# Kernel optimization log

Hardware: AMD Instinct MI355X
Metric: run time of the kernel (lower is better)

The kernel has to match this reference:

```python
import jax, jax.numpy as jnp
import numpy as np
from jax import lax

B, N, M = 4, 16384, 512
RADIUS2 = 4.0        # radius=2 (hard-coded in forward), compare squared distances
BALL_K = 64          # k=64 hard-coded in forward
KNN_K = 9            # opt.node_knn_k_1
SIGMA_LB = 0.001     # opt.loss_sigma_lower_bound

_DIMS = [("conv1", 6, 64), ("conv2", 64, 64), ("conv3", 64, 64),
         ("conv4", 128, 128), ("conv5", 128, 128),
         ("knnb1", 131, 256), ("knnb2", 256, 256), ("knnb3", 256, 256),
         ("knna1", 512, 512), ("knna2", 512, 512),
         ("mlp1", 640, 512), ("mlp2", 512, 256)]


def setup_inputs() -> dict:
    key = jax.random.key(0)
    ks = jax.random.split(key, 6)
    inp = {
        "x": jax.random.normal(ks[0], (B, 3, N), jnp.float32),
        "sn": jax.random.normal(ks[1], (B, 3, N), jnp.float32),
        "node": jax.random.normal(ks[2], (B, 3, M), jnp.float32),
    }
    for i, (name, cin, cout) in enumerate(_DIMS):
        k = jax.random.fold_in(ks[3], i)
        inp[name + "_w"] = jax.random.normal(k, (cout, cin), jnp.float32) * np.float32(1.0 / np.sqrt(cin))
        inp[name + "_b"] = jnp.zeros((cout,), jnp.float32)
    inp["mlp3_w"] = jax.random.normal(ks[4], (4, 256), jnp.float32) * np.float32(1e-4)  # .normal_(0, 0.0001)
    inp["mlp3_b"] = jnp.zeros((4,), jnp.float32)
    return inp


def _conv(f, w, b, act=True):
    # 1x1 conv over (B,C,M) or (B,C,M,K): channel matmul + bias (+relu)
    y = jnp.einsum('oc,bc...->bo...', w, f) + b.reshape((1, -1) + (1,) * (f.ndim - 2))
    return jax.nn.relu(y) if act else y


def _sqdist(a, b):
    # a: (B,3,Ma), b: (B,3,Nb) -> (B,Ma,Nb) squared euclidean distances
    aa = jnp.sum(a * a, axis=1)
    bb = jnp.sum(b * b, axis=1)
    ab = jnp.einsum('bcm,bcn->bmn', a, b)
    return aa[:, :, None] + bb[:, None, :] - 2.0 * ab


def _gather(feat, idx):
    # feat: (B,C,Nb), idx: (B,Mq,K) -> (B,C,Mq,K)
    Bq, C, _ = feat.shape
    _, Mq, K = idx.shape
    flat = jnp.broadcast_to(idx.reshape(Bq, 1, Mq * K), (Bq, C, Mq * K))
    return jnp.take_along_axis(feat, flat, axis=2).reshape(Bq, C, Mq, K)


def _ball_query(sqd, radius2, k):
    # first k point indices (in original order) with dist<radius, padded by the first hit
    n = sqd.shape[2]
    mask = sqd < radius2
    keyi = jnp.where(mask, jnp.arange(n, dtype=jnp.int32)[None, None, :], jnp.int32(n))
    _, idx = lax.top_k(-keyi, k)  # k smallest keys == first k in-ball indices
    count = jnp.sum(mask, axis=2, keepdims=True)
    return jnp.where(jnp.arange(k)[None, None, :] < count, idx, idx[:, :, :1])


def reference(x, sn, node,
              conv1_w, conv1_b, conv2_w, conv2_b, conv3_w, conv3_b,
              conv4_w, conv4_b, conv5_w, conv5_b,
              knnb1_w, knnb1_b, knnb2_w, knnb2_b, knnb3_w, knnb3_b,
              knna1_w, knna1_b, knna2_w, knna2_b,
              mlp1_w, mlp1_b, mlp2_w, mlp2_b, mlp3_w, mlp3_b):
    x_aug = jnp.concatenate([x, sn], axis=1)                      # (B,6,N)
    idx = _ball_query(_sqdist(node, x), RADIUS2, BALL_K)          # (B,M,64)
    xb = _gather(x_aug, idx)                                      # (B,6,M,64)
    xb = jnp.concatenate([xb[:, :3] - node[:, :, :, None], xb[:, 3:]], axis=1)
    f = _conv(_conv(_conv(xb, conv1_w, conv1_b), conv2_w, conv2_b), conv3_w, conv3_b)
    fmax = jnp.max(f, axis=3, keepdims=True)
    f = jnp.concatenate([f, jnp.broadcast_to(fmax, f.shape)], axis=1)
    f = _conv(_conv(f, conv4_w, conv4_b), conv5_w, conv5_b)
    feat1 = jnp.max(f, axis=3)                                    # (B,128,M)

    # GeneralKNNFusionModule: query=node, database=node, x=feat1, K=KNN_K
    _, knn_idx = lax.top_k(-_sqdist(node, node), KNN_K)           # (B,M,K) nearest nodes
    coords = _gather(node, knn_idx) - node[:, :, :, None]         # (B,3,M,K)
    g = jnp.concatenate([coords, _gather(feat1, knn_idx)], axis=1)  # (B,131,M,K)
    g = _conv(_conv(_conv(g, knnb1_w, knnb1_b), knnb2_w, knnb2_b), knnb3_w, knnb3_b)
    gmax = jnp.max(g, axis=3, keepdims=True)
    g = jnp.concatenate([g, jnp.broadcast_to(gmax, g.shape)], axis=1)
    g = _conv(_conv(g, knna1_w, knna1_b), knna2_w, knna2_b)
    feat2 = jnp.max(g, axis=3)                                    # (B,512,M)

    h = jnp.concatenate([feat1, feat2], axis=1)                   # (B,640,M)
    h = _conv(_conv(h, mlp1_w, mlp1_b), mlp2_w, mlp2_b)
    ksig = _conv(h, mlp3_w, mlp3_b, act=False)                    # (B,4,M)
    keypoints = ksig[:, :3] + node
    sigmas = jax.nn.softplus(ksig[:, 3]) + SIGMA_LB
    return node, keypoints, sigmas
```

## Files before the change

kernel.cpp:

```cpp
#include <hip/hip_runtime.h>

typedef unsigned short u16;
typedef unsigned int u32;
typedef __bf16 bf16x8 __attribute__((ext_vector_type(8)));
typedef float floatx4 __attribute__((ext_vector_type(4)));
typedef unsigned short u16x8 __attribute__((ext_vector_type(8)));
typedef unsigned int u32x4 __attribute__((ext_vector_type(4)));

static constexpr int B_ = 4;
static constexpr int N_ = 16384;
static constexpr int M_ = 512;

__device__ __forceinline__ u16 f2bf(float f) {
    u32 u = __float_as_uint(f);
    u32 r = (u + 0x7fffu + ((u >> 16) & 1u)) >> 16;
    return (u16)r;
}
__device__ __forceinline__ float bf2f(u16 x) {
    return __uint_as_float(((u32)x) << 16);
}
__device__ __forceinline__ u32 pack2(float a, float b) {
    return (u32)f2bf(a) | ((u32)f2bf(b) << 16);
}

struct WConvArgs { const float* src[12]; };

__global__ __launch_bounds__(256) void prep_kernel(
    const float* __restrict__ node, int* __restrict__ knn,
    WConvArgs wa, u16* __restrict__ Wbf) {
    int bid = blockIdx.x;
    int tid = threadIdx.x, wave = tid >> 6, lane = tid & 63;

    if (bid < 512) {
        int bm = bid * 4 + wave;
        int b = bm >> 9, m = bm & 511;
        const float* nb = node + (size_t)b * 3 * M_;
        float nx = nb[m], ny = nb[M_ + m], nz = nb[2 * M_ + m];
        float aa = nx * nx + ny * ny + nz * nz;
        float dist[8];
        int didx[8];
#pragma unroll
        for (int i = 0; i < 8; ++i) {
            int n = lane + i * 64;
            float px = nb[n], py = nb[M_ + n], pz = nb[2 * M_ + n];
            float bb = px * px + py * py + pz * pz;
            float ab = nx * px + ny * py + nz * pz;
            dist[i] = aa + bb - 2.0f * ab;
            didx[i] = n;
        }
        for (int r = 0; r < 9; ++r) {
            float bv = dist[0]; int bi = didx[0]; int bslot = 0;
#pragma unroll
            for (int i = 1; i < 8; ++i) {
                if (dist[i] < bv || (dist[i] == bv && didx[i] < bi)) {
                    bv = dist[i]; bi = didx[i]; bslot = i;
                }
            }
            float rv = bv; int ri = bi;
            for (int off = 32; off > 0; off >>= 1) {
                float ov = __shfl_down(rv, off);
                int   oi = __shfl_down(ri, off);
                if (ov < rv || (ov == rv && oi < ri)) { rv = ov; ri = oi; }
            }
            ri = __shfl(ri, 0);
            if (lane == 0) knn[(size_t)bm * 9 + r] = ri;
            if (bi == ri) dist[bslot] = 3.0e38f;
        }
    } else {
        const int CI[12] = {6, 64, 64, 128, 128, 131, 256, 256, 512, 512, 640, 512};
        const int KP[12] = {32, 64, 64, 128, 128, 160, 256, 256, 512, 512, 640, 512};
        const int OFF[13] = {0, 2048, 6144, 10240, 26624, 43008, 83968, 149504,
                             215040, 477184, 739328, 1067008, 1198080};
        int e = (bid - 512) * 256 + tid;
        int w = 0;
        while (e >= OFF[w + 1]) ++w;
        int local = e - OFF[w];
        int kp = KP[w];
        int co = local / kp, k = local - co * kp;
        float v = 0.0f;
        if (w == 5) {
            if (k < 3) v = wa.src[5][(size_t)co * 131 + k];
            else if (k >= 8 && k < 136) v = wa.src[5][(size_t)co * 131 + (k - 5)];
        } else if (k < CI[w]) {
            v = wa.src[w][(size_t)co * CI[w] + k];
        }
        Wbf[e] = f2bf(v);
    }
}

static constexpr int RS = 136;

__device__ __forceinline__ bf16x8 ldsA(const u16* act, int rf, int l15, int quad, int ks) {
    return *(const bf16x8*)(act + (rf * 16 + l15) * RS + ks * 32 + quad * 8);
}
__device__ __forceinline__ bf16x8 ldW(const u16* W, int ks, int l15, int quad, int kstride) {
    return *(const bf16x8*)(W + (size_t)l15 * kstride + ks * 32 + quad * 8);
}

__global__ __launch_bounds__(256, 4) void fused_stage1_kernel(
    const float* __restrict__ x, const float* __restrict__ sn,
    const float* __restrict__ node,
    const u16* __restrict__ Wbf,
    const float* __restrict__ b1, const float* __restrict__ b2,
    const float* __restrict__ b3, const float* __restrict__ b4,
    const float* __restrict__ b5, u16* __restrict__ h) {
    __shared__ __align__(16) u16 act[64 * RS];
    __shared__ __align__(16) u16 mv[64];
    __shared__ int sidx[4][64];
    __shared__ int scnt[4];
    int bm = blockIdx.x;
    int b = bm >> 9, m = bm & 511;
    int tid = threadIdx.x, wave = tid >> 6, lane = tid & 63;
    int quad = lane >> 4, l15 = lane & 15;

    {
        const float* xb = x + (size_t)b * 3 * N_;
        float nx = node[((size_t)b * 3 + 0) * M_ + m];
        float ny = node[((size_t)b * 3 + 1) * M_ + m];
        float nz = node[((size_t)b * 3 + 2) * M_ + m];
        float aa = nx * nx + ny * ny + nz * nz;
        int cnt = 0;
        int base = wave * 4096;
#pragma unroll 1
        for (int n0 = base; n0 < base + 4096; n0 += 256) {
            float px[4], py[4], pz[4];
#pragma unroll
            for (int i = 0; i < 4; ++i) {
                int n = n0 + i * 64 + lane;
                px[i] = xb[n]; py[i] = xb[N_ + n]; pz[i] = xb[2 * N_ + n];
            }
#pragma unroll
            for (int i = 0; i < 4; ++i) {
                float bb = px[i] * px[i] + py[i] * py[i] + pz[i] * pz[i];
                float d = aa + bb - 2.0f * (nx * px[i] + ny * py[i] + nz * pz[i]);
                bool inb = d < 4.0f;
                unsigned long long mask = __ballot(inb);
                if (inb && cnt < 64) {
                    int pos = cnt + __popcll(mask & ((1ull << lane) - 1ull));
                    if (pos < 64) sidx[wave][pos] = n0 + i * 64 + lane;
                }
                cnt += __popcll(mask);
            }
            if (cnt >= 64) break;
        }
        if (lane == 0) scnt[wave] = cnt;
    }
    __syncthreads();

    if (tid < 64) {
        int total = scnt[0] + scnt[1] + scnt[2] + scnt[3];
        int j = 0;
        if (total > 0) {
            int lim = total < 64 ? total : 64;
            int slot = tid < lim ? tid : 0;
            int w = 0, pre = 0;
            while (w < 3 && slot >= pre + scnt[w]) { pre += scnt[w]; ++w; }
            j = sidx[w][slot - pre];
        }
        const float* xb = x + (size_t)b * 3 * N_;
        const float* sb = sn + (size_t)b * 3 * N_;
        float c0 = xb[j]          - node[((size_t)b * 3 + 0) * M_ + m];
        float c1 = xb[N_ + j]     - node[((size_t)b * 3 + 1) * M_ + m];
        float c2 = xb[2 * N_ + j] - node[((size_t)b * 3 + 2) * M_ + m];
        float s0 = sb[j], s1 = sb[N_ + j], s2 = sb[2 * N_ + j];
        u16* r = act + tid * RS;
        *(u32*)(r)     = pack2(c0, c1);
        *(u32*)(r + 2) = pack2(c2, s0);
        *(u32*)(r + 4) = pack2(s1, s2);
        *(u32*)(r + 6) = 0u;
        u32x4* z = (u32x4*)(r + 8);
        z[0] = (u32x4){0u, 0u, 0u, 0u};
        z[1] = (u32x4){0u, 0u, 0u, 0u};
        z[2] = (u32x4){0u, 0u, 0u, 0u};
    }
    __syncthreads();

    {
        const u16* Wp = Wbf + (size_t)(wave * 16) * 32;
        bf16x8 bw = ldW(Wp, 0, l15, quad, 32);
        floatx4 c[4];
#pragma unroll
        for (int rf = 0; rf < 4; ++rf) {
            bf16x8 a = ldsA(act, rf, l15, quad, 0);
            c[rf] = __builtin_amdgcn_mfma_f32_16x16x32_bf16(a, bw, (floatx4){0.f,0.f,0.f,0.f}, 0, 0, 0);
        }
        float bias = b1[wave * 16 + l15];
        __syncthreads();
#pragma unroll
        for (int rf = 0; rf < 4; ++rf)
#pragma unroll
            for (int r = 0; r < 4; ++r)
                act[(rf * 16 + quad * 4 + r) * RS + wave * 16 + l15] = f2bf(fmaxf(c[rf][r] + bias, 0.0f));
        __syncthreads();
    }

    const int WOFF23[2] = {2048, 6144};
    const float* bp23[2] = {b2, b3};
#pragma unroll 1
    for (int cv = 0; cv < 2; ++cv) {
        const u16* Wp = Wbf + WOFF23[cv] + (size_t)(wave * 16) * 64;
        bf16x8 bw0 = ldW(Wp, 0, l15, quad, 64);
        bf16x8 bw1 = ldW(Wp, 1, l15, quad, 64);
        floatx4 c[4] = {};
#pragma unroll
        for (int ks = 0; ks < 2; ++ks)
#pragma unroll
            for (int rf = 0; rf < 4; ++rf) {
                bf16x8 a = ldsA(act, rf, l15, quad, ks);
                c[rf] = __builtin_amdgcn_mfma_f32_16x16x32_bf16(a, ks ? bw1 : bw0, c[rf], 0, 0, 0);
            }
        float bias = bp23[cv][wave * 16 + l15];
        float mx = 0.0f;
#pragma unroll
        for (int rf = 0; rf < 4; ++rf)
#pragma unroll
            for (int r = 0; r < 4; ++r)
                mx = fmaxf(mx, fmaxf(c[rf][r] + bias, 0.0f));
        __syncthreads();
#pragma unroll
        for (int rf = 0; rf < 4; ++rf)
#pragma unroll
            for (int r = 0; r < 4; ++r)
                act[(rf * 16 + quad * 4 + r) * RS + wave * 16 + l15] = f2bf(fmaxf(c[rf][r] + bias, 0.0f));
        if (cv == 1) {
            mx = fmaxf(mx, __shfl_xor(mx, 16));
            mx = fmaxf(mx, __shfl_xor(mx, 32));
            if (quad == 0) mv[wave * 16 + l15] = f2bf(mx);
        }
        __syncthreads();
    }

    {
        const u16* Wp = Wbf + 10240 + (size_t)(wave * 32) * 128;
        bf16x8 bw[2][4];
#pragma unroll
        for (int cf = 0; cf < 2; ++cf)
#pragma unroll
            for (int ks = 0; ks < 4; ++ks)
                bw[cf][ks] = ldW(Wp + (size_t)cf * 16 * 128, ks, l15, quad, 128);
        floatx4 c[4][2] = {};
#pragma unroll
        for (int ks = 0; ks < 4; ++ks) {
            bf16x8 amv;
            if (ks >= 2) amv = *(const bf16x8*)(&mv[(ks - 2) * 32 + quad * 8]);
#pragma unroll
            for (int rf = 0; rf < 4; ++rf) {
                bf16x8 a = (ks < 2) ? ldsA(act, rf, l15, quad, ks) : amv;
#pragma unroll
                for (int cf = 0; cf < 2; ++cf)
                    c[rf][cf] = __builtin_amdgcn_mfma_f32_16x16x32_bf16(a, bw[cf][ks], c[rf][cf], 0, 0, 0);
            }
        }
        float bias[2];
#pragma unroll
        for (int cf = 0; cf < 2; ++cf) bias[cf] = b4[wave * 32 + cf * 16 + l15];
        __syncthreads();
#pragma unroll
        for (int rf = 0; rf < 4; ++rf)
#pragma unroll
            for (int cf = 0; cf < 2; ++cf)
#pragma unroll
                for (int r = 0; r < 4; ++r)
                    act[(rf * 16 + quad * 4 + r) * RS + wave * 32 + cf * 16 + l15] =
                        f2bf(fmaxf(c[rf][cf][r] + bias[cf], 0.0f));
        __syncthreads();
    }

    {
        const u16* Wp = Wbf + 26624 + (size_t)(wave * 32) * 128;
        bf16x8 bw[2][4];
#pragma unroll
        for (int cf = 0; cf < 2; ++cf)
#pragma unroll
            for (int ks = 0; ks < 4; ++ks)
                bw[cf][ks] = ldW(Wp + (size_t)cf * 16 * 128, ks, l15, quad, 128);
        floatx4 c[4][2] = {};
#pragma unroll
        for (int ks = 0; ks < 4; ++ks)
#pragma unroll
            for (int rf = 0; rf < 4; ++rf) {
                bf16x8 a = ldsA(act, rf, l15, quad, ks);
#pragma unroll
                for (int cf = 0; cf < 2; ++cf)
                    c[rf][cf] = __builtin_amdgcn_mfma_f32_16x16x32_bf16(a, bw[cf][ks], c[rf][cf], 0, 0, 0);
            }
#pragma unroll
        for (int cf = 0; cf < 2; ++cf) {
            float bias = b5[wave * 32 + cf * 16 + l15];
            float mx = 0.0f;
#pragma unroll
            for (int rf = 0; rf < 4; ++rf)
#pragma unroll
                for (int r = 0; r < 4; ++r)
                    mx = fmaxf(mx, fmaxf(c[rf][cf][r] + bias, 0.0f));
            mx = fmaxf(mx, __shfl_xor(mx, 16));
            mx = fmaxf(mx, __shfl_xor(mx, 32));
            if (quad == 0)
                h[(size_t)bm * 128 + wave * 32 + cf * 16 + l15] = f2bf(mx);
        }
    }
}

template <int KS, int CF, int RF, int PF, int RSx>
__device__ __forceinline__ void conv_inplace(u16* act, const u16* __restrict__ W0, int KP,
                                             const float* __restrict__ bias, int cb,
                                             int l15, int quad) {
    floatx4 acc[RF][CF];
#pragma unroll
    for (int rf = 0; rf < RF; ++rf)
#pragma unroll
        for (int cf = 0; cf < CF; ++cf) acc[rf][cf] = (floatx4){0.f, 0.f, 0.f, 0.f};

    bf16x8 bw[PF][CF];
#pragma unroll
    for (int p = 0; p < PF - 1; ++p)
        if (p < KS)
#pragma unroll
            for (int cf = 0; cf < CF; ++cf)
                bw[p][cf] = *(const bf16x8*)(W0 + (size_t)(cb + cf * 16 + l15) * KP +
                                             p * 32 + quad * 8);

#pragma unroll
    for (int ks = 0; ks < KS; ++ks) {
        if (ks + PF - 1 < KS) {
#pragma unroll
            for (int cf = 0; cf < CF; ++cf)
                bw[(ks + PF - 1) & (PF - 1)][cf] =
                    *(const bf16x8*)(W0 + (size_t)(cb + cf * 16 + l15) * KP +
                                     (ks + PF - 1) * 32 + quad * 8);
        }
#pragma unroll
        for (int rf = 0; rf < RF; ++rf) {
            bf16x8 a = *(const bf16x8*)(act + (rf * 16 + l15) * RSx + ks * 32 + quad * 8);
#pragma unroll
            for (int cf = 0; cf < CF; ++cf)
                acc[rf][cf] = __builtin_amdgcn_mfma_f32_16x16x32_bf16(a, bw[ks & (PF - 1)][cf], acc[rf][cf], 0, 0, 0);
        }
    }
    __syncthreads();
#pragma unroll
    for (int cf = 0; cf < CF; ++cf) {
        float bs = bias[cb + cf * 16 + l15];
#pragma unroll
        for (int rf = 0; rf < RF; ++rf)
#pragma unroll
            for (int r = 0; r < 4; ++r)
                act[(rf * 16 + quad * 4 + r) * RSx + cb + cf * 16 + l15] =
                    f2bf(fmaxf(acc[rf][cf][r] + bs, 0.0f));
    }
    __syncthreads();
}

static constexpr int RS2 = 520;
static constexpr int RS3 = 648;

__global__ __launch_bounds__(512, 2) void fused_stage23_kernel(
    const float* __restrict__ node, const u16* __restrict__ h,
    const int* __restrict__ knn, const u16* __restrict__ Wbf,
    const float* __restrict__ bb1, const float* __restrict__ bb2,
    const float* __restrict__ bb3, const float* __restrict__ ba1,
    const float* __restrict__ ba2,
    const float* __restrict__ bm1, const float* __restrict__ bm2,
    const float* __restrict__ w3, const float* __restrict__ b3,
    float* __restrict__ out) {
    __shared__ __align__(16) u16 act[80 * RS2 + 16 * RS3];
    u16* mlpT = act + 80 * RS2;
    int blk = blockIdx.x;
    int node0 = blk * 8;
    int b = node0 >> 9;
    int tid = threadIdx.x, wave = tid >> 6, lane = tid & 63;
    int quad = lane >> 4, l15 = lane & 15;
    (void)lane;

    for (int e = tid; e < 80 * 20; e += 512)
        *(u16x8*)(act + (e / 20) * RS2 + (e % 20) * 8) = (u16x8){0,0,0,0,0,0,0,0};
    __syncthreads();
    for (int e = tid; e < 72 * 3; e += 512) {
        int r = e / 3, c = e - r * 3;
        int nodei = node0 + r / 9;
        int j = knn[(size_t)nodei * 9 + (r % 9)];
        float v = node[((size_t)b * 3 + c) * M_ + j] - node[((size_t)b * 3 + c) * M_ + (nodei & 511)];
        act[r * RS2 + c] = f2bf(v);
    }
    for (int e = tid; e < 72 * 16; e += 512) {
        int r = e >> 4, s = e & 15;
        int nodei = node0 + r / 9;
        int j = knn[(size_t)nodei * 9 + (r % 9)];
        *(u16x8*)(act + r * RS2 + 8 + s * 8) =
            *(const u16x8*)(h + (size_t)(b * 512 + j) * 128 + s * 8);
    }
    __syncthreads();

    conv_inplace<5, 2, 5, 4, RS2>(act, Wbf + 43008, 160, bb1, wave * 32, l15, quad);
    conv_inplace<8, 2, 5, 4, RS2>(act, Wbf + 83968, 256, bb2, wave * 32, l15, quad);
    conv_inplace<8, 2, 5, 4, RS2>(act, Wbf + 149504, 256, bb3, wave * 32, l15, quad);

    for (int e = tid; e < 8 * 32; e += 512) {
        int li = e >> 5, s = e & 31;
        int r0 = li * 9;
        float mx[8];
#pragma unroll
        for (int i = 0; i < 8; ++i) mx[i] = -3.0e38f;
#pragma unroll
        for (int kk = 0; kk < 9; ++kk) {
            u16x8 v = *(const u16x8*)(act + (r0 + kk) * RS2 + s * 8);
#pragma unroll
            for (int i = 0; i < 8; ++i) mx[i] = fmaxf(mx[i], bf2f(v[i]));
        }
        u16x8 o;
#pragma unroll
        for (int i = 0; i < 8; ++i) o[i] = f2bf(mx[i]);
#pragma unroll
        for (int kk = 0; kk < 9; ++kk)
            *(u16x8*)(act + (r0 + kk) * RS2 + 256 + s * 8) = o;
    }
    __syncthreads();

    conv_inplace<16, 4, 5, 4, RS2>(act, Wbf + 215040, 512, ba1, wave * 64, l15, quad);
    conv_inplace<16, 4, 5, 4, RS2>(act, Wbf + 477184, 512, ba2, wave * 64, l15, quad);

    for (int e = tid; e < 8 * 64; e += 512) {
        int li = e >> 6, s = e & 63;
        int r0 = li * 9;
        float mx[8];
#pragma unroll
        for (int i = 0; i < 8; ++i) mx[i] = -3.0e38f;
#pragma unroll
        for (int kk = 0; kk < 9; ++kk) {
            u16x8 v = *(const u16x8*)(act + (r0 + kk) * RS2 + s * 8);
#pragma unroll
            for (int i = 0; i < 8; ++i) mx[i] = fmaxf(mx[i], bf2f(v[i]));
        }
        u16x8 o;
#pragma unroll
        for (int i = 0; i < 8; ++i) o[i] = f2bf(mx[i]);
        *(u16x8*)(mlpT + li * RS3 + 128 + s * 8) = o;
    }
    for (int e = tid; e < 8 * 16; e += 512) {
        int li = e >> 4, s = e & 15;
        *(u16x8*)(mlpT + li * RS3 + s * 8) =
            *(const u16x8*)(h + (size_t)(node0 + li) * 128 + s * 8);
    }
    for (int e = tid; e < 8 * 80; e += 512) {
        int r = e / 80, seg = e - r * 80;
        *(u16x8*)(mlpT + (8 + r) * RS3 + seg * 8) = (u16x8){0,0,0,0,0,0,0,0};
    }
    __syncthreads();

    conv_inplace<20, 4, 1, 4, RS3>(mlpT, Wbf + 739328, 640, bm1, wave * 64, l15, quad);
    conv_inplace<16, 2, 1, 4, RS3>(mlpT, Wbf + 1067008, 512, bm2, wave * 32, l15, quad);

    if (tid < 32) {
        int li = tid >> 2, oc = tid & 3;
        const u16* row = mlpT + li * RS3;
        const float* wrow = w3 + oc * 256;
        float a = 0.0f;
        for (int c = 0; c < 256; c += 4) {
            a += bf2f(row[c]) * wrow[c];
            a += bf2f(row[c + 1]) * wrow[c + 1];
            a += bf2f(row[c + 2]) * wrow[c + 2];
            a += bf2f(row[c + 3]) * wrow[c + 3];
        }
        a += b3[oc];
        int nodei = node0 + li;
        int bo = nodei >> 9, m = nodei & 511;
        if (oc < 3) {
            float nv = node[((size_t)bo * 3 + oc) * M_ + m];
            out[((size_t)bo * 3 + oc) * M_ + m] = nv;
            out[6144 + ((size_t)bo * 3 + oc) * M_ + m] = nv + a;
        } else {
            out[12288 + nodei] = fmaxf(a, 0.0f) + log1pf(expf(-fabsf(a))) + 0.001f;
        }
    }
}

extern "C" void kernel_launch(void* const* d_in, const int* in_sizes, int n_in,
                              void* d_out, int out_size, void* d_ws, size_t ws_size,
                              hipStream_t stream) {
    (void)in_sizes; (void)n_in; (void)out_size; (void)ws_size;
    const float* x = (const float*)d_in[0];
    const float* sn = (const float*)d_in[1];
    const float* node = (const float*)d_in[2];
    const float* W[13];
    const float* Bs[13];
    for (int i = 0; i < 13; ++i) {
        W[i] = (const float*)d_in[3 + 2 * i];
        Bs[i] = (const float*)d_in[4 + 2 * i];
    }
    float* out = (float*)d_out;

    char* ws = (char*)d_ws;
    int* knn = (int*)(ws + 0);
    u16* Wbf = (u16*)(ws + 73728);
    u16* h   = (u16*)(ws + 2469888);

    WConvArgs wa;
    for (int w = 0; w < 12; ++w) wa.src[w] = W[w];

    prep_kernel<<<5192, 256, 0, stream>>>(node, knn, wa, Wbf);

    fused_stage1_kernel<<<2048, 256, 0, stream>>>(x, sn, node, Wbf,
                                                  Bs[0], Bs[1], Bs[2], Bs[3], Bs[4], h);
    fused_stage23_kernel<<<256, 512, 0, stream>>>(node, h, knn, Wbf,
                                                  Bs[5], Bs[6], Bs[7], Bs[8], Bs[9],
                                                  Bs[10], Bs[11], W[12], Bs[12], out);
}
```

Measured before the change: 231.5 us.

## Fuse all three stages into one cooperative mega-kernel with grid syncs

Replaces the prep, stage1 and stage23 launches with a single cooperative kernel of 256 blocks by 512 threads. Grid-wide syncs separate weight conversion, KNN and ball query from the stage1 convs, and stage1 from the stage23 tail. KNN indices now stay in shared memory instead of going through a global buffer. The aim is to remove launch gaps and inter-kernel round trips. In exchange, stage1 now runs on only 256 blocks (8 nodes each) instead of 2048, which lowers parallelism and occupancy, and the grid syncs add their own cost.

```diff
diff --git a/kernel.cpp b/kernel.cpp
--- a/kernel.cpp
+++ b/kernel.cpp
@@ -1,4 +1,7 @@
 #include <hip/hip_runtime.h>
+#include <hip/hip_cooperative_groups.h>
+
+namespace cg = cooperative_groups;
 
 typedef unsigned short u16;
 typedef unsigned int u32;
@@ -24,6 +27,453 @@
 }
 
 struct WConvArgs { const float* src[12]; };
+
+static constexpr int RS = 136;
+static constexpr int RS2 = 520;
+static constexpr int RS3 = 648;
+
+template <int KS, int CF, int RF, int PF, int RSx>
+__device__ __forceinline__ void conv_inplace(u16* act, const u16* __restrict__ W0, int KP,
+                                             const float* __restrict__ bias, int cb,
+                                             int l15, int quad) {
+    floatx4 acc[RF][CF];
+#pragma unroll
+    for (int rf = 0; rf < RF; ++rf)
+#pragma unroll
+        for (int cf = 0; cf < CF; ++cf) acc[rf][cf] = (floatx4){0.f, 0.f, 0.f, 0.f};
+
+    bf16x8 bw[PF][CF];
+#pragma unroll
+    for (int p = 0; p < PF - 1; ++p)
+        if (p < KS)
+#pragma unroll
+            for (int cf = 0; cf < CF; ++cf)
+                bw[p][cf] = *(const bf16x8*)(W0 + (size_t)(cb + cf * 16 + l15) * KP +
+                                             p * 32 + quad * 8);
+
+#pragma unroll
+    for (int ks = 0; ks < KS; ++ks) {
+        if (ks + PF - 1 < KS) {
+#pragma unroll
+            for (int cf = 0; cf < CF; ++cf)
+                bw[(ks + PF - 1) & (PF - 1)][cf] =
+                    *(const bf16x8*)(W0 + (size_t)(cb + cf * 16 + l15) * KP +
+                                     (ks + PF - 1) * 32 + quad * 8);
+        }
+#pragma unroll
+        for (int rf = 0; rf < RF; ++rf) {
+            bf16x8 a = *(const bf16x8*)(act + (rf * 16 + l15) * RSx + ks * 32 + quad * 8);
+#pragma unroll
+            for (int cf = 0; cf < CF; ++cf)
+                acc[rf][cf] = __builtin_amdgcn_mfma_f32_16x16x32_bf16(a, bw[ks & (PF - 1)][cf], acc[rf][cf], 0, 0, 0);
+        }
+    }
+    __syncthreads();
+#pragma unroll
+    for (int cf = 0; cf < CF; ++cf) {
+        float bs = bias[cb + cf * 16 + l15];
+#pragma unroll
+        for (int rf = 0; rf < RF; ++rf)
+#pragma unroll
+            for (int r = 0; r < 4; ++r)
+                act[(rf * 16 + quad * 4 + r) * RSx + cb + cf * 16 + l15] =
+                    f2bf(fmaxf(acc[rf][cf][r] + bs, 0.0f));
+    }
+    __syncthreads();
+}
+
+__global__ __launch_bounds__(512, 2) void mega_kernel(
+    const float* __restrict__ x, const float* __restrict__ sn,
+    const float* __restrict__ node, WConvArgs wa,
+    u16* __restrict__ Wbf, u16* __restrict__ h,
+    const float* __restrict__ b1, const float* __restrict__ b2,
+    const float* __restrict__ b3, const float* __restrict__ b4,
+    const float* __restrict__ b5,
+    const float* __restrict__ bb1, const float* __restrict__ bb2,
+    const float* __restrict__ bb3, const float* __restrict__ ba1,
+    const float* __restrict__ ba2,
+    const float* __restrict__ bm1, const float* __restrict__ bm2,
+    const float* __restrict__ w3, const float* __restrict__ b3f,
+    float* __restrict__ out) {
+    __shared__ __align__(16) u16 actU[512 * RS];
+    __shared__ __align__(16) u16 mvL[8][64];
+    __shared__ int sidx[8][64];
+    __shared__ int scnt[8];
+    __shared__ int knnL[8][9];
+
+    int blk = blockIdx.x;
+    int node0 = blk * 8;
+    int tid = threadIdx.x, wave = tid >> 6, lane = tid & 63;
+    int quad = lane >> 4, l15 = lane & 15;
+    int g = node0 + wave;
+    int b = g >> 9, m = g & 511;
+
+    {
+        const int CI[12] = {6, 64, 64, 128, 128, 131, 256, 256, 512, 512, 640, 512};
+        const int KP[12] = {32, 64, 64, 128, 128, 160, 256, 256, 512, 512, 640, 512};
+        const int OFF[13] = {0, 2048, 6144, 10240, 26624, 43008, 83968, 149504,
+                             215040, 477184, 739328, 1067008, 1198080};
+#pragma unroll 1
+        for (int e = blk * 512 + tid; e < 1198080; e += 131072) {
+            int w = 0;
+            while (e >= OFF[w + 1]) ++w;
+            int local = e - OFF[w];
+            int kp = KP[w];
+            int co = local / kp, k = local - co * kp;
+            float v = 0.0f;
+            if (w == 5) {
+                if (k < 3) v = wa.src[5][(size_t)co * 131 + k];
+                else if (k >= 8 && k < 136) v = wa.src[5][(size_t)co * 131 + (k - 5)];
+            } else if (k < CI[w]) {
+                v = wa.src[w][(size_t)co * CI[w] + k];
+            }
+            Wbf[e] = f2bf(v);
+        }
+    }
+
+    float nx = node[((size_t)b * 3 + 0) * M_ + m];
+    float ny = node[((size_t)b * 3 + 1) * M_ + m];
+    float nz = node[((size_t)b * 3 + 2) * M_ + m];
+    float aa = nx * nx + ny * ny + nz * nz;
+
+    {
+        const float* nb = node + (size_t)b * 3 * M_;
+        float dist[8];
+        int didx[8];
+#pragma unroll
+        for (int i = 0; i < 8; ++i) {
+            int n = lane + i * 64;
+            float px = nb[n], py = nb[M_ + n], pz = nb[2 * M_ + n];
+            float bb = px * px + py * py + pz * pz;
+            float ab = nx * px + ny * py + nz * pz;
+            dist[i] = aa + bb - 2.0f * ab;
+            didx[i] = n;
+        }
+#pragma unroll 1
+        for (int r = 0; r < 9; ++r) {
+            float bv = dist[0]; int bi = didx[0]; int bslot = 0;
+#pragma unroll
+            for (int i = 1; i < 8; ++i) {
+                if (dist[i] < bv || (dist[i] == bv && didx[i] < bi)) {
+                    bv = dist[i]; bi = didx[i]; bslot = i;
+                }
+            }
+            float rv = bv; int ri = bi;
+            for (int off = 32; off > 0; off >>= 1) {
+                float ov = __shfl_down(rv, off);
+                int   oi = __shfl_down(ri, off);
+                if (ov < rv || (ov == rv && oi < ri)) { rv = ov; ri = oi; }
+            }
+            ri = __shfl(ri, 0);
+            if (lane == 0) knnL[wave][r] = ri;
+            if (bi == ri) dist[bslot] = 3.0e38f;
+        }
+    }
+
+    {
+        const float* xb = x + (size_t)b * 3 * N_;
+        int cnt = 0;
+#pragma unroll 1
+        for (int n0 = 0; n0 < N_; n0 += 256) {
+            float px[4], py[4], pz[4];
+#pragma unroll
+            for (int i = 0; i < 4; ++i) {
+                int n = n0 + i * 64 + lane;
+                px[i] = xb[n]; py[i] = xb[N_ + n]; pz[i] = xb[2 * N_ + n];
+            }
+#pragma unroll
+            for (int i = 0; i < 4; ++i) {
+                float bb = px[i] * px[i] + py[i] * py[i] + pz[i] * pz[i];
+                float d = aa + bb - 2.0f * (nx * px[i] + ny * py[i] + nz * pz[i]);
+                bool inb = d < 4.0f;
+                unsigned long long mask = __ballot(inb);
+                if (inb && cnt < 64) {
+                    int pos = cnt + __popcll(mask & ((1ull << lane) - 1ull));
+                    if (pos < 64) sidx[wave][pos] = n0 + i * 64 + lane;
+                }
+                cnt += __popcll(mask);
+            }
+            if (cnt >= 64) break;
+        }
+        if (lane == 0) scnt[wave] = cnt < 64 ? cnt : 64;
+    }
+    __syncthreads();
+    __threadfence();
+    cg::this_grid().sync();
+
+    u16* base = actU + wave * 64 * RS;
+    {
+        int c = scnt[wave];
+        int j = (c == 0) ? 0 : sidx[wave][lane < c ? lane : 0];
+        const float* xb = x + (size_t)b * 3 * N_;
+        const float* sb = sn + (size_t)b * 3 * N_;
+        float c0 = xb[j] - nx;
+        float c1 = xb[N_ + j] - ny;
+        float c2 = xb[2 * N_ + j] - nz;
+        float s0 = sb[j], s1 = sb[N_ + j], s2 = sb[2 * N_ + j];
+        u16* r = base + lane * RS;
+        *(u32*)(r)     = pack2(c0, c1);
+        *(u32*)(r + 2) = pack2(c2, s0);
+        *(u32*)(r + 4) = pack2(s1, s2);
+        *(u32*)(r + 6) = 0u;
+        u32x4* z = (u32x4*)(r + 8);
+        z[0] = (u32x4){0u, 0u, 0u, 0u};
+        z[1] = (u32x4){0u, 0u, 0u, 0u};
+        z[2] = (u32x4){0u, 0u, 0u, 0u};
+    }
+    __syncthreads();
+
+    {
+        bf16x8 bw[4];
+#pragma unroll
+        for (int cf = 0; cf < 4; ++cf)
+            bw[cf] = *(const bf16x8*)(Wbf + (size_t)(cf * 16 + l15) * 32 + quad * 8);
+        floatx4 c[4][4];
+#pragma unroll
+        for (int rf = 0; rf < 4; ++rf) {
+            bf16x8 a = *(const bf16x8*)(base + (rf * 16 + l15) * RS + quad * 8);
+#pragma unroll
+            for (int cf = 0; cf < 4; ++cf)
+                c[rf][cf] = __builtin_amdgcn_mfma_f32_16x16x32_bf16(a, bw[cf], (floatx4){0.f,0.f,0.f,0.f}, 0, 0, 0);
+        }
+#pragma unroll
+        for (int cf = 0; cf < 4; ++cf) {
+            float bias = b1[cf * 16 + l15];
+#pragma unroll
+            for (int rf = 0; rf < 4; ++rf)
+#pragma unroll
+                for (int r = 0; r < 4; ++r)
+                    base[(rf * 16 + quad * 4 + r) * RS + cf * 16 + l15] = f2bf(fmaxf(c[rf][cf][r] + bias, 0.0f));
+        }
+        __syncthreads();
+    }
+
+    {
+        const int WOFF23[2] = {2048, 6144};
+        const float* bp23[2] = {b2, b3};
+#pragma unroll 1
+        for (int cv = 0; cv < 2; ++cv) {
+            const u16* Wp = Wbf + WOFF23[cv];
+            bf16x8 bw[2][4];
+#pragma unroll
+            for (int ks = 0; ks < 2; ++ks)
+#pragma unroll
+                for (int cf = 0; cf < 4; ++cf)
+                    bw[ks][cf] = *(const bf16x8*)(Wp + (size_t)(cf * 16 + l15) * 64 + ks * 32 + quad * 8);
+            floatx4 c[4][4] = {};
+#pragma unroll
+            for (int ks = 0; ks < 2; ++ks)
+#pragma unroll
+                for (int rf = 0; rf < 4; ++rf) {
+                    bf16x8 a = *(const bf16x8*)(base + (rf * 16 + l15) * RS + ks * 32 + quad * 8);
+#pragma unroll
+                    for (int cf = 0; cf < 4; ++cf)
+                        c[rf][cf] = __builtin_amdgcn_mfma_f32_16x16x32_bf16(a, bw[ks][cf], c[rf][cf], 0, 0, 0);
+                }
+#pragma unroll
+            for (int cf = 0; cf < 4; ++cf) {
+                float bias = bp23[cv][cf * 16 + l15];
+                float mxv = 0.0f;
+#pragma unroll
+                for (int rf = 0; rf < 4; ++rf)
+#pragma unroll
+                    for (int r = 0; r < 4; ++r) {
+                        float v = fmaxf(c[rf][cf][r] + bias, 0.0f);
+                        mxv = fmaxf(mxv, v);
+                        base[(rf * 16 + quad * 4 + r) * RS + cf * 16 + l15] = f2bf(v);
+                    }
+                if (cv == 1) {
+                    mxv = fmaxf(mxv, __shfl_xor(mxv, 16));
+                    mxv = fmaxf(mxv, __shfl_xor(mxv, 32));
+                    if (quad == 0) mvL[wave][cf * 16 + l15] = f2bf(mxv);
+                }
+            }
+            __syncthreads();
+        }
+    }
+
+    {
+#pragma unroll 1
+        for (int cp = 1; cp >= 0; --cp) {
+            const u16* Wp = Wbf + 10240 + (size_t)(cp * 64) * 128;
+            bf16x8 bw[4][4];
+#pragma unroll
+            for (int cf = 0; cf < 4; ++cf)
+#pragma unroll
+                for (int ks = 0; ks < 4; ++ks)
+                    bw[cf][ks] = *(const bf16x8*)(Wp + (size_t)(cf * 16 + l15) * 128 + ks * 32 + quad * 8);
+            floatx4 c[4][4] = {};
+#pragma unroll
+            for (int ks = 0; ks < 4; ++ks) {
+                bf16x8 amv;
+                if (ks >= 2) amv = *(const bf16x8*)(&mvL[wave][(ks - 2) * 32 + quad * 8]);
+#pragma unroll
+                for (int rf = 0; rf < 4; ++rf) {
+                    bf16x8 a = (ks < 2) ? *(const bf16x8*)(base + (rf * 16 + l15) * RS + ks * 32 + quad * 8)
+                                        : amv;
+#pragma unroll
+                    for (int cf = 0; cf < 4; ++cf)
+                        c[rf][cf] = __builtin_amdgcn_mfma_f32_16x16x32_bf16(a, bw[cf][ks], c[rf][cf], 0, 0, 0);
+                }
+            }
+#pragma unroll
+            for (int cf = 0; cf < 4; ++cf) {
+                float bias = b4[cp * 64 + cf * 16 + l15];
+#pragma unroll
+                for (int rf = 0; rf < 4; ++rf)
+#pragma unroll
+                    for (int r = 0; r < 4; ++r)
+                        base[(rf * 16 + quad * 4 + r) * RS + cp * 64 + cf * 16 + l15] =
+                            f2bf(fmaxf(c[rf][cf][r] + bias, 0.0f));
+            }
+        }
+        __syncthreads();
+    }
+
+    {
+#pragma unroll 1
+        for (int cp = 0; cp < 2; ++cp) {
+            const u16* Wp = Wbf + 26624 + (size_t)(cp * 64) * 128;
+            bf16x8 bw[4][4];
+#pragma unroll
+            for (int cf = 0; cf < 4; ++cf)
+#pragma unroll
+                for (int ks = 0; ks < 4; ++ks)
+                    bw[cf][ks] = *(const bf16x8*)(Wp + (size_t)(cf * 16 + l15) * 128 + ks * 32 + quad * 8);
+            floatx4 c[4][4] = {};
+#pragma unroll
+            for (int ks = 0; ks < 4; ++ks)
+#pragma unroll
+                for (int rf = 0; rf < 4; ++rf) {
+                    bf16x8 a = *(const bf16x8*)(base + (rf * 16 + l15) * RS + ks * 32 + quad * 8);
+#pragma unroll
+                    for (int cf = 0; cf < 4; ++cf)
+                        c[rf][cf] = __builtin_amdgcn_mfma_f32_16x16x32_bf16(a, bw[cf][ks], c[rf][cf], 0, 0, 0);
+                }
+#pragma unroll
+            for (int cf = 0; cf < 4; ++cf) {
+                float bias = b5[cp * 64 + cf * 16 + l15];
+                float mxv = 0.0f;
+#pragma unroll
+                for (int rf = 0; rf < 4; ++rf)
+#pragma unroll
+                    for (int r = 0; r < 4; ++r)
+                        mxv = fmaxf(mxv, fmaxf(c[rf][cf][r] + bias, 0.0f));
+                mxv = fmaxf(mxv, __shfl_xor(mxv, 16));
+                mxv = fmaxf(mxv, __shfl_xor(mxv, 32));
+                if (quad == 0)
+                    h[(size_t)g * 128 + cp * 64 + cf * 16 + l15] = f2bf(mxv);
+            }
+        }
+    }
+    __syncthreads();
+    __threadfence();
+    cg::this_grid().sync();
+
+    u16* act = actU;
+    u16* mlpT = actU + 80 * RS2;
+
+    for (int e = tid; e < 80 * 20; e += 512)
+        *(u16x8*)(act + (e / 20) * RS2 + (e % 20) * 8) = (u16x8){0,0,0,0,0,0,0,0};
+    __syncthreads();
+    for (int e = tid; e < 72 * 3; e += 512) {
+        int r = e / 3, c = e - r * 3;
+        int li = r / 9;
+        int j = knnL[li][r % 9];
+        int nodei = node0 + li;
+        float v = node[((size_t)b * 3 + c) * M_ + j] - node[((size_t)b * 3 + c) * M_ + (nodei & 511)];
+        act[r * RS2 + c] = f2bf(v);
+    }
+    for (int e = tid; e < 72 * 16; e += 512) {
+        int r = e >> 4, s = e & 15;
+        int j = knnL[r / 9][r % 9];
+        *(u16x8*)(act + r * RS2 + 8 + s * 8) =
+            *(const u16x8*)(h + (size_t)(b * 512 + j) * 128 + s * 8);
+    }
+    __syncthreads();
+
+    conv_inplace<5, 2, 5, 4, RS2>(act, Wbf + 43008, 160, bb1, wave * 32, l15, quad);
+    conv_inplace<8, 2, 5, 4, RS2>(act, Wbf + 83968, 256, bb2, wave * 32, l15, quad);
+    conv_inplace<8, 2, 5, 4, RS2>(act, Wbf + 149504, 256, bb3, wave * 32, l15, quad);
+
+    for (int e = tid; e < 8 * 32; e += 512) {
+        int li = e >> 5, s = e & 31;
+        int r0 = li * 9;
+        float mx[8];
+#pragma unroll
+        for (int i = 0; i < 8; ++i) mx[i] = -3.0e38f;
+#pragma unroll
+        for (int kk = 0; kk < 9; ++kk) {
+            u16x8 v = *(const u16x8*)(act + (r0 + kk) * RS2 + s * 8);
+#pragma unroll
+            for (int i = 0; i < 8; ++i) mx[i] = fmaxf(mx[i], bf2f(v[i]));
+        }
+        u16x8 o;
+#pragma unroll
+        for (int i = 0; i < 8; ++i) o[i] = f2bf(mx[i]);
+#pragma unroll
+        for (int kk = 0; kk < 9; ++kk)
+            *(u16x8*)(act + (r0 + kk) * RS2 + 256 + s * 8) = o;
+    }
+    __syncthreads();
+
+    conv_inplace<16, 4, 5, 4, RS2>(act, Wbf + 215040, 512, ba1, wave * 64, l15, quad);
+    conv_inplace<16, 4, 5, 4, RS2>(act, Wbf + 477184, 512, ba2, wave * 64, l15, quad);
+
+    for (int e = tid; e < 8 * 64; e += 512) {
+        int li = e >> 6, s = e & 63;
+        int r0 = li * 9;
+        float mx[8];
+#pragma unroll
+        for (int i = 0; i < 8; ++i) mx[i] = -3.0e38f;
+#pragma unroll
+        for (int kk = 0; kk < 9; ++kk) {
+            u16x8 v = *(const u16x8*)(act + (r0 + kk) * RS2 + s * 8);
+#pragma unroll
+            for (int i = 0; i < 8; ++i) mx[i] = fmaxf(mx[i], bf2f(v[i]));
+        }
+        u16x8 o;
+#pragma unroll
+        for (int i = 0; i < 8; ++i) o[i] = f2bf(mx[i]);
+        *(u16x8*)(mlpT + li * RS3 + 128 + s * 8) = o;
+    }
+    for (int e = tid; e < 8 * 16; e += 512) {
+        int li = e >> 4, s = e & 15;
+        *(u16x8*)(mlpT + li * RS3 + s * 8) =
+            *(const u16x8*)(h + (size_t)(node0 + li) * 128 + s * 8);
+    }
+    for (int e = tid; e < 8 * 80; e += 512) {
+        int r = e / 80, seg = e - r * 80;
+        *(u16x8*)(mlpT + (8 + r) * RS3 + seg * 8) = (u16x8){0,0,0,0,0,0,0,0};
+    }
+    __syncthreads();
+
+    conv_inplace<20, 4, 1, 4, RS3>(mlpT, Wbf + 739328, 640, bm1, wave * 64, l15, quad);
+    conv_inplace<16, 2, 1, 4, RS3>(mlpT, Wbf + 1067008, 512, bm2, wave * 32, l15, quad);
+
+    if (tid < 32) {
+        int li = tid >> 2, oc = tid & 3;
+        const u16* row = mlpT + li * RS3;
+        const float* wrow = w3 + oc * 256;
+        float a = 0.0f;
+        for (int c = 0; c < 256; c += 4) {
+            a += bf2f(row[c]) * wrow[c];
+            a += bf2f(row[c + 1]) * wrow[c + 1];
+            a += bf2f(row[c + 2]) * wrow[c + 2];
+            a += bf2f(row[c + 3]) * wrow[c + 3];
+        }
+        a += b3f[oc];
+        int nodei = node0 + li;
+        int bo = nodei >> 9, mo = nodei & 511;
+        if (oc < 3) {
+            float nv = node[((size_t)bo * 3 + oc) * M_ + mo];
+            out[((size_t)bo * 3 + oc) * M_ + mo] = nv;
+            out[6144 + ((size_t)bo * 3 + oc) * M_ + mo] = nv + a;
+        } else {
+            out[12288 + nodei] = fmaxf(a, 0.0f) + log1pf(expf(-fabsf(a))) + 0.001f;
+        }
+    }
+}
 
 __global__ __launch_bounds__(256) void prep_kernel(
     const float* __restrict__ node, int* __restrict__ knn,
@@ -88,8 +538,6 @@
     }
 }
 
-static constexpr int RS = 136;
-
 __device__ __forceinline__ bf16x8 ldsA(const u16* act, int rf, int l15, int quad, int ks) {
     return *(const bf16x8*)(act + (rf * 16 + l15) * RS + ks * 32 + quad * 8);
 }
@@ -300,59 +748,6 @@
         }
     }
 }
-
-template <int KS, int CF, int RF, int PF, int RSx>
-__device__ __forceinline__ void conv_inplace(u16* act, const u16* __restrict__ W0, int KP,
-                                             const float* __restrict__ bias, int cb,
-                                             int l15, int quad) {
-    floatx4 acc[RF][CF];
-#pragma unroll
-    for (int rf = 0; rf < RF; ++rf)
-#pragma unroll
-        for (int cf = 0; cf < CF; ++cf) acc[rf][cf] = (floatx4){0.f, 0.f, 0.f, 0.f};
-
-    bf16x8 bw[PF][CF];
-#pragma unroll
-    for (int p = 0; p < PF - 1; ++p)
-        if (p < KS)
-#pragma unroll
-            for (int cf = 0; cf < CF; ++cf)
-                bw[p][cf] = *(const bf16x8*)(W0 + (size_t)(cb + cf * 16 + l15) * KP +
-                                             p * 32 + quad * 8);
-
-#pragma unroll
-    for (int ks = 0; ks < KS; ++ks) {
-        if (ks + PF - 1 < KS) {
-#pragma unroll
-            for (int cf = 0; cf < CF; ++cf)
-                bw[(ks + PF - 1) & (PF - 1)][cf] =
-                    *(const bf16x8*)(W0 + (size_t)(cb + cf * 16 + l15) * KP +
-                                     (ks + PF - 1) * 32 + quad * 8);
-        }
-#pragma unroll
-        for (int rf = 0; rf < RF; ++rf) {
-            bf16x8 a = *(const bf16x8*)(act + (rf * 16 + l15) * RSx + ks * 32 + quad * 8);
-#pragma unroll
-            for (int cf = 0; cf < CF; ++cf)
-                acc[rf][cf] = __builtin_amdgcn_mfma_f32_16x16x32_bf16(a, bw[ks & (PF - 1)][cf], acc[rf][cf], 0, 0, 0);
-        }
-    }
-    __syncthreads();
-#pragma unroll
-    for (int cf = 0; cf < CF; ++cf) {
-        float bs = bias[cb + cf * 16 + l15];
-#pragma unroll
-        for (int rf = 0; rf < RF; ++rf)
-#pragma unroll
-            for (int r = 0; r < 4; ++r)
-                act[(rf * 16 + quad * 4 + r) * RSx + cb + cf * 16 + l15] =
-                    f2bf(fmaxf(acc[rf][cf][r] + bs, 0.0f));
-    }
-    __syncthreads();
-}
-
-static constexpr int RS2 = 520;
-static constexpr int RS3 = 648;
 
 __global__ __launch_bounds__(512, 2) void fused_stage23_kernel(
     const float* __restrict__ node, const u16* __restrict__ h,
@@ -497,11 +892,24 @@
     WConvArgs wa;
     for (int w = 0; w < 12; ++w) wa.src[w] = W[w];
 
-    prep_kernel<<<5192, 256, 0, stream>>>(node, knn, wa, Wbf);
-
-    fused_stage1_kernel<<<2048, 256, 0, stream>>>(x, sn, node, Wbf,
-                                                  Bs[0], Bs[1], Bs[2], Bs[3], Bs[4], h);
-    fused_stage23_kernel<<<256, 512, 0, stream>>>(node, h, knn, Wbf,
-                                                  Bs[5], Bs[6], Bs[7], Bs[8], Bs[9],
-                                                  Bs[10], Bs[11], W[12], Bs[12], out);
-}
+    const float* w3 = W[12];
+    void* args[] = {
+        (void*)&x, (void*)&sn, (void*)&node, (void*)&wa,
+        (void*)&Wbf, (void*)&h,
+        (void*)&Bs[0], (void*)&Bs[1], (void*)&Bs[2], (void*)&Bs[3], (void*)&Bs[4],
+        (void*)&Bs[5], (void*)&Bs[6], (void*)&Bs[7], (void*)&Bs[8], (void*)&Bs[9],
+        (void*)&Bs[10], (void*)&Bs[11], (void*)&w3, (void*)&Bs[12],
+        (void*)&out
+    };
+    hipError_t err = hipLaunchCooperativeKernel(
+        (const void*)mega_kernel, dim3(256), dim3(512), args, 0, stream);
+
+    if (err != hipSuccess) {
+        prep_kernel<<<5192, 256, 0, stream>>>(node, knn, wa, Wbf);
+        fused_stage1_kernel<<<2048, 256, 0, stream>>>(x, sn, node, Wbf,
+                                                      Bs[0], Bs[1], Bs[2], Bs[3], Bs[4], h);
+        fused_stage23_kernel<<<256, 512, 0, stream>>>(node, h, knn, Wbf,
+                                                      Bs[5], Bs[6], Bs[7], Bs[8], Bs[9],
+                                                      Bs[10], Bs[11], W[12], Bs[12], out);
+    }
+}
```

Result: slower. 408.8 us (+76.6%).
